# Performance work log

Measured on AMD Instinct MI355X. Metric: run time of the kernel, lower is better.

The kernel has to match this reference:

```python
import jax, jax.numpy as jnp
import numpy as np

B, E, DIM = 8, 2048, 512
KERNEL = 8
DECAY_CONSTANT = 1.0


def _forward(x, weight, bias, decay_value):
    # x: (B, E, S) with S == dim; weight: (K, S); bias: (S,); decay_value: (2, 1)
    K, dim = weight.shape
    Bb, Ee, S = x.shape
    i = jnp.arange(dim)[:, None]
    j = jnp.arange(dim)[None, :]
    # decayed upper-triangular weight: W[k, i, j] = weight[k, j] * dv^((j-i)/c) for j >= i
    dv = jnp.clip(decay_value[1, 0], 0.9, 1.0)
    d = dv ** ((j - i).astype(x.dtype) / DECAY_CONSTANT)  # (S, S)
    W = jnp.where(j >= i, weight[:, None, :] * d[None], jnp.zeros((), x.dtype))  # (K, S, S)
    p = K - 1
    padded = jnp.pad(x, ((0, 0), (p, p), (0, 0)))  # zero-pad sequence axis
    # shifted stack: stacked[b, k, e] = x[b, e + k - (K-1)] (zeros out of range) -> causal taps
    stacked = jnp.stack([padded[:, k:Ee + k] for k in range(K)], axis=1)  # (B, K, E, S)
    out = jnp.einsum('bkei,kij->bej', stacked, W) + bias
    return out


def setup_inputs() -> dict:
    key = jax.random.key(0)
    k1, k2 = jax.random.split(key)
    x = jax.random.normal(k1, (B, E, DIM), dtype=jnp.float32)
    weight = jax.random.normal(k2, (KERNEL, DIM), dtype=jnp.float32)
    bias = jnp.zeros((DIM,), dtype=jnp.float32)
    decay_value = jnp.ones((2, 1), dtype=jnp.float32)
    return {"x": x, "weight": weight, "bias": bias, "decay_value": decay_value}


def reference(x, weight, bias, decay_value):
    return _forward(x, weight, bias, decay_value)
```

## Files before the change

kernel.cpp:

```cpp
#include <hip/hip_runtime.h>


#define B_    8
#define E_    2048
#define DIM_  512
#define K_    8
#define TILE_E 32
#define NROWS  (TILE_E + K_ - 1)

__global__ __launch_bounds__(256) void krl_fused(
    const float* __restrict__ x,
    const float* __restrict__ weight,
    const float* __restrict__ bias,
    const float* __restrict__ decay,
    float* __restrict__ out)
{
    __shared__ float yls[NROWS][DIM_];

    const int tile = blockIdx.x;
    const int b    = blockIdx.y;
    const int e0   = tile * TILE_E;

    const int t    = threadIdx.x;
    const int lane = t & 63;
    const int wave = t >> 6;

    float dv = decay[1];
    dv = fminf(fmaxf(dv, 0.9f), 1.0f);
    const float dv2 = dv * dv;
    const float dv4 = dv2 * dv2;
    const float dv8 = dv4 * dv4;

    for (int r = wave; r < NROWS; r += 4) {
        const int eg  = e0 - (K_ - 1) + r;
        const int egc = eg < 0 ? 0 : eg;
        const float4* xp = (const float4*)(x + ((size_t)b * E_ + egc) * DIM_ + lane * 8);
        float4 a0 = xp[0];
        float4 a1 = xp[1];
        if (eg < 0) {
            a0 = make_float4(0.f, 0.f, 0.f, 0.f);
            a1 = a0;
        }
        const float xv[8] = {a0.x, a0.y, a0.z, a0.w, a1.x, a1.y, a1.z, a1.w};

        float tl[8];
        tl[0] = xv[0];
        #pragma unroll
        for (int m = 1; m < 8; ++m) tl[m] = fmaf(dv, tl[m - 1], xv[m]);

        float v  = tl[7];
        float ap = dv8;
        #pragma unroll
        for (int off = 1; off < 64; off <<= 1) {
            float up = __shfl_up(v, off, 64);
            if (lane >= off) v = fmaf(ap, up, v);
            ap *= ap;
        }
        float carry = __shfl_up(v, 1, 64);
        if (lane == 0) carry = 0.f;
        float dp = dv;
        #pragma unroll
        for (int m = 0; m < 8; ++m) { tl[m] = fmaf(dp, carry, tl[m]); dp *= dv; }

        float4* yp = (float4*)(&yls[r][lane * 8]);
        yp[0] = make_float4(tl[0], tl[1], tl[2], tl[3]);
        yp[1] = make_float4(tl[4], tl[5], tl[6], tl[7]);
    }

    const int jf = (t & 127) * 4;
    float4 w[K_];
    #pragma unroll
    for (int k = 0; k < K_; ++k) w[k] = *(const float4*)(weight + k * DIM_ + jf);
    const float4 bi = *(const float4*)(bias + jf);

    __syncthreads();

    const int g = t >> 7;
    for (int te = g; te < TILE_E; te += 2) {
        float4 acc = bi;
        #pragma unroll
        for (int k = 0; k < K_; ++k) {
            const float4 yv = *(const float4*)(&yls[te + k][jf]);
            acc.x = fmaf(w[k].x, yv.x, acc.x);
            acc.y = fmaf(w[k].y, yv.y, acc.y);
            acc.z = fmaf(w[k].z, yv.z, acc.z);
            acc.w = fmaf(w[k].w, yv.w, acc.w);
        }
        *(float4*)(out + ((size_t)b * E_ + e0 + te) * DIM_ + jf) = acc;
    }
}

extern "C" void kernel_launch(void* const* d_in, const int* in_sizes, int n_in,
                              void* d_out, int out_size, void* d_ws, size_t ws_size,
                              hipStream_t stream) {
    const float* x      = (const float*)d_in[0];
    const float* weight = (const float*)d_in[1];
    const float* bias   = (const float*)d_in[2];
    const float* decay  = (const float*)d_in[3];
    float* out = (float*)d_out;

    dim3 grid(E_ / TILE_E, B_);
    dim3 block(256);
    krl_fused<<<grid, block, 0, stream>>>(x, weight, bias, decay, out);
}
```

Baseline: 96.83 us.

## Restructure decay scan as segmented per-row scan with sliding register window

The x tile is now loaded cooperatively and coalesced into padded shared memory, with a row stride of 516 to avoid bank conflicts. The decay prefix scan is done by 16-lane groups per row: each lane scans 128 elements serially, and only two cross-segment shuffles are needed instead of a six-step shuffle scan over 64 lanes. The output stage keeps a sliding window of 8 rows in registers, so each step reads one new row from LDS instead of eight. The cost is a longer serial dependency chain per lane, lanes left idle for rows past 39, and more register pressure.

```diff
diff --git a/kernel.cpp b/kernel.cpp
--- a/kernel.cpp
+++ b/kernel.cpp
@@ -1,73 +1,86 @@
 #include <hip/hip_runtime.h>
 
 
-#define B_    8
-#define E_    2048
-#define DIM_  512
-#define K_    8
+#define B_     8
+#define E_     2048
+#define DIM_   512
+#define K_     8
 #define TILE_E 32
 #define NROWS  (TILE_E + K_ - 1)
+#define LSTR   516
+#define NF4    (NROWS * (DIM_ / 4))
 
-__global__ __launch_bounds__(256) void krl_fused(
+__global__ __launch_bounds__(256) void krl_t(
     const float* __restrict__ x,
     const float* __restrict__ weight,
     const float* __restrict__ bias,
     const float* __restrict__ decay,
     float* __restrict__ out)
 {
-    __shared__ float yls[NROWS][DIM_];
+    __shared__ float yls[NROWS * LSTR];
 
-    const int tile = blockIdx.x;
-    const int b    = blockIdx.y;
-    const int e0   = tile * TILE_E;
+    const int t  = threadIdx.x;
+    const int b  = blockIdx.y;
+    const int e0 = blockIdx.x * TILE_E;
 
-    const int t    = threadIdx.x;
-    const int lane = t & 63;
-    const int wave = t >> 6;
+    const int ebase = e0 - (K_ - 1);
+    for (int i = t; i < NF4; i += 256) {
+        const int r  = i >> 7;
+        const int f4 = i & 127;
+        const int eg = ebase + r;
+        float4 v = make_float4(0.f, 0.f, 0.f, 0.f);
+        if (eg >= 0)
+            v = *(const float4*)(x + ((size_t)b * E_ + eg) * DIM_ + f4 * 4);
+        *(float4*)(&yls[r * LSTR + f4 * 4]) = v;
+    }
 
     float dv = decay[1];
     dv = fminf(fmaxf(dv, 0.9f), 1.0f);
-    const float dv2 = dv * dv;
-    const float dv4 = dv2 * dv2;
-    const float dv8 = dv4 * dv4;
+    const float d1 = dv, d2 = dv * dv, d3 = d2 * dv, d4 = d2 * d2;
+    float d128 = d4;
+    d128 *= d128; d128 *= d128; d128 *= d128; d128 *= d128; d128 *= d128;
+    const float d256 = d128 * d128;
 
-    for (int r = wave; r < NROWS; r += 4) {
-        const int eg  = e0 - (K_ - 1) + r;
-        const int egc = eg < 0 ? 0 : eg;
-        const float4* xp = (const float4*)(x + ((size_t)b * E_ + egc) * DIM_ + lane * 8);
-        float4 a0 = xp[0];
-        float4 a1 = xp[1];
-        if (eg < 0) {
-            a0 = make_float4(0.f, 0.f, 0.f, 0.f);
-            a1 = a0;
+    __syncthreads();
+
+    const int lane = t & 63, wave = t >> 6;
+    const int r16 = lane & 15, seg = lane >> 4;
+    const int row = wave * 16 + r16;
+    if (row < NROWS) {
+        float* sp = &yls[row * LSTR + seg * 128];
+
+        float E = 0.f;
+        #pragma unroll 8
+        for (int q = 0; q < 32; ++q) {
+            const float4 v = *(const float4*)(sp + 4 * q);
+            const float p = fmaf(d3, v.x, fmaf(d2, v.y, fmaf(d1, v.z, v.w)));
+            E = fmaf(d4, E, p);
         }
-        const float xv[8] = {a0.x, a0.y, a0.z, a0.w, a1.x, a1.y, a1.z, a1.w};
 
-        float tl[8];
-        tl[0] = xv[0];
-        #pragma unroll
-        for (int m = 1; m < 8; ++m) tl[m] = fmaf(dv, tl[m - 1], xv[m]);
+        float S = E;
+        float u1 = __shfl_up(S, 16, 64); if (seg >= 1) S = fmaf(d128, u1, S);
+        float u2 = __shfl_up(S, 32, 64); if (seg >= 2) S = fmaf(d256, u2, S);
+        float C = __shfl_up(S, 16, 64);  if (seg == 0) C = 0.f;
 
-        float v  = tl[7];
-        float ap = dv8;
-        #pragma unroll
-        for (int off = 1; off < 64; off <<= 1) {
-            float up = __shfl_up(v, off, 64);
-            if (lane >= off) v = fmaf(ap, up, v);
-            ap *= ap;
+        float prev = C;
+        #pragma unroll 8
+        for (int q = 0; q < 32; ++q) {
+            const float4 v = *(const float4*)(sp + 4 * q);
+            const float p01   = fmaf(d1, v.x, v.y);
+            const float p012  = fmaf(d1, p01, v.z);
+            const float p0123 = fmaf(d1, p012, v.w);
+            float4 yv;
+            yv.x = fmaf(d1, prev, v.x);
+            yv.y = fmaf(d2, prev, p01);
+            yv.z = fmaf(d3, prev, p012);
+            yv.w = fmaf(d4, prev, p0123);
+            prev = yv.w;
+            *(float4*)(sp + 4 * q) = yv;
         }
-        float carry = __shfl_up(v, 1, 64);
-        if (lane == 0) carry = 0.f;
-        float dp = dv;
-        #pragma unroll
-        for (int m = 0; m < 8; ++m) { tl[m] = fmaf(dp, carry, tl[m]); dp *= dv; }
-
-        float4* yp = (float4*)(&yls[r][lane * 8]);
-        yp[0] = make_float4(tl[0], tl[1], tl[2], tl[3]);
-        yp[1] = make_float4(tl[4], tl[5], tl[6], tl[7]);
     }
 
-    const int jf = (t & 127) * 4;
+    const int j  = t & 127, h = t >> 7;
+    const int jf = j * 4;
     float4 w[K_];
     #pragma unroll
     for (int k = 0; k < K_; ++k) w[k] = *(const float4*)(weight + k * DIM_ + jf);
@@ -75,18 +88,27 @@
 
     __syncthreads();
 
-    const int g = t >> 7;
-    for (int te = g; te < TILE_E; te += 2) {
+    const int te0 = h * 16;
+    float4 win[K_];
+    #pragma unroll
+    for (int k = 0; k < 7; ++k)
+        win[k] = *(const float4*)(&yls[(te0 + k) * LSTR + jf]);
+
+    #pragma unroll
+    for (int i = 0; i < 16; ++i) {
+        const int te = te0 + i;
+        win[7] = *(const float4*)(&yls[(te + 7) * LSTR + jf]);
         float4 acc = bi;
         #pragma unroll
         for (int k = 0; k < K_; ++k) {
-            const float4 yv = *(const float4*)(&yls[te + k][jf]);
-            acc.x = fmaf(w[k].x, yv.x, acc.x);
-            acc.y = fmaf(w[k].y, yv.y, acc.y);
-            acc.z = fmaf(w[k].z, yv.z, acc.z);
-            acc.w = fmaf(w[k].w, yv.w, acc.w);
+            acc.x = fmaf(w[k].x, win[k].x, acc.x);
+            acc.y = fmaf(w[k].y, win[k].y, acc.y);
+            acc.z = fmaf(w[k].z, win[k].z, acc.z);
+            acc.w = fmaf(w[k].w, win[k].w, acc.w);
         }
         *(float4*)(out + ((size_t)b * E_ + e0 + te) * DIM_ + jf) = acc;
+        #pragma unroll
+        for (int k = 0; k < 7; ++k) win[k] = win[k + 1];
     }
 }
 
@@ -101,5 +123,5 @@
 
     dim3 grid(E_ / TILE_E, B_);
     dim3 block(256);
-    krl_fused<<<grid, block, 0, stream>>>(x, weight, bias, decay, out);
+    krl_t<<<grid, block, 0, stream>>>(x, weight, bias, decay, out);
 }
```

New measurement: 91.08 us. 5.9% less time.
